# Optimization experiments

Hardware: AMD Instinct MI355X
Metric: run time of the kernel (lower is better)

The kernel has to match this reference:

```python
import jax, jax.numpy as jnp
import numpy as np

H = 512; W = 512; PH = 16; PW = 16; Q = 3; JITTER = 1e-06
NH = H // PH; NW = W // PW; P = NH * NW
B = 64


def setup_inputs() -> dict:
    key = jax.random.key(0)
    k0, k1, k2, k3, k4 = jax.random.split(key, 5)
    x = jax.random.normal(k0, (B, H, W), dtype=jnp.float32)
    logits = jax.random.normal(k1, (P, Q), dtype=jnp.float32)
    mu = jax.random.normal(k2, (P, Q, 2), dtype=jnp.float32) * 0.3
    sigma = jnp.exp(jax.random.normal(k3, (P, Q, 2), dtype=jnp.float32) * 0.3)
    bias = jax.random.normal(k4, (P, PH, PW), dtype=jnp.float32)
    return {"x": x, "logits": logits, "mu": mu, "sigma": sigma, "bias": bias}


def _make_S(logits, mu, sigma):
    # logits: (P,Q), mu/sigma: (P,Q,2) -> S: (P,PH,PW)
    w = jax.nn.softmax(logits, axis=-1)            # (P,Q)
    fy = jnp.fft.fftfreq(PH).astype(jnp.float32)   # (PH,)
    fx = jnp.fft.fftfreq(PW).astype(jnp.float32)   # (PW,)
    mu_y = mu[..., 0][:, :, None, None]            # (P,Q,1,1)
    mu_x = mu[..., 1][:, :, None, None]
    sg_y = sigma[..., 0][:, :, None, None]
    sg_x = sigma[..., 1][:, :, None, None]
    fy_b = fy[None, None, :, None]                 # (1,1,PH,1)
    fx_b = fx[None, None, None, :]                 # (1,1,1,PW)
    g1 = jnp.exp(-0.5 * (((fy_b - mu_y) / sg_y) ** 2 + ((fx_b - mu_x) / sg_x) ** 2))
    g2 = jnp.exp(-0.5 * (((fy_b + mu_y) / sg_y) ** 2 + ((fx_b + mu_x) / sg_x) ** 2))
    # weighted sum over mixture components Q
    S = jnp.einsum('pq,pqhw->phw', w, g1 + g2) + JITTER
    return S


def reference(x, logits, mu, sigma, bias):
    # x: (B,H,W) -> (B,H,W)
    S = _make_S(logits, mu, sigma)                                  # (P,PH,PW)
    x_p = x.reshape(B, NH, PH, NW, PW)
    x_p = x_p.transpose(1, 3, 0, 2, 4).reshape(P, B, PH, PW)        # (P,B,PH,PW)
    Xf = jnp.fft.fftn(x_p, axes=(-2, -1))                           # complex64
    y_p = jnp.fft.ifftn(Xf * S[:, None, :, :], axes=(-2, -1)).real  # (P,B,PH,PW)
    y_p = y_p + bias[:, None, :, :]
    y = y_p.reshape(NH, NW, B, PH, PW)
    y = y.transpose(2, 0, 3, 1, 4).reshape(B, H, W)
    return y
```

## Files before the change

kernel.cpp:

```cpp
#include <hip/hip_runtime.h>
#include <math.h>

#define HH 512
#define WW 512
#define PHH 16
#define PWW 16
#define QQ 3
#define NHH 32
#define NWW 32
#define PP 1024
#define BB 64

__device__ __forceinline__ void wfence() {
  asm volatile("" ::: "memory");
  __builtin_amdgcn_sched_barrier(0);
}

template <int SGN, int T>
__device__ __forceinline__ void bfly(float& ar, float& ai, float& br, float& bi) {
  float tr, ti;
  if constexpr (T == 0) {
    tr = br;
    ti = bi;
  } else if constexpr (T == 4) {
    if constexpr (SGN > 0) { tr = bi;  ti = -br; }
    else                   { tr = -bi; ti = br;  }
  } else if constexpr (T == 2) {
    constexpr float c = 0.70710678118654752440f;
    if constexpr (SGN > 0) { tr = c * (br + bi); ti = c * (bi - br); }
    else                   { tr = c * (br - bi); ti = c * (bi + br); }
  } else if constexpr (T == 6) {
    constexpr float c = 0.70710678118654752440f;
    if constexpr (SGN > 0) { tr = c * (bi - br);  ti = -c * (br + bi); }
    else                   { tr = -c * (br + bi); ti = c * (br - bi);  }
  } else {
    constexpr float c1 = 0.92387953251128675613f;
    constexpr float s1 = 0.38268343236508977173f;
    constexpr float wr = (T == 1) ? c1 : (T == 3) ? s1 : (T == 5) ? -s1 : -c1;
    constexpr float wi0 = (T == 1) ? -s1 : (T == 3) ? -c1 : (T == 5) ? -c1 : -s1;
    constexpr float wi = (SGN > 0) ? wi0 : -wi0;
    tr = br * wr - bi * wi;
    ti = br * wi + bi * wr;
  }
  br = ar - tr;
  bi = ai - ti;
  ar = ar + tr;
  ai = ai + ti;
}

template <int SGN>
__device__ __forceinline__ void fft16(float re[16], float im[16]) {
#define SW_(a, b)                              \
  { float t = re[a]; re[a] = re[b]; re[b] = t; \
    t = im[a]; im[a] = im[b]; im[b] = t; }
  SW_(1, 8) SW_(2, 4) SW_(3, 12) SW_(5, 10) SW_(7, 14) SW_(11, 13)
#undef SW_
#define BF_(a, b, T) bfly<SGN, T>(re[a], im[a], re[b], im[b]);
  BF_(0, 1, 0) BF_(2, 3, 0) BF_(4, 5, 0) BF_(6, 7, 0)
  BF_(8, 9, 0) BF_(10, 11, 0) BF_(12, 13, 0) BF_(14, 15, 0)
  BF_(0, 2, 0) BF_(1, 3, 4) BF_(4, 6, 0) BF_(5, 7, 4)
  BF_(8, 10, 0) BF_(9, 11, 4) BF_(12, 14, 0) BF_(13, 15, 4)
  BF_(0, 4, 0) BF_(1, 5, 2) BF_(2, 6, 4) BF_(3, 7, 6)
  BF_(8, 12, 0) BF_(9, 13, 2) BF_(10, 14, 4) BF_(11, 15, 6)
  BF_(0, 8, 0) BF_(1, 9, 1) BF_(2, 10, 2) BF_(3, 11, 3)
  BF_(4, 12, 4) BF_(5, 13, 5) BF_(6, 14, 6) BF_(7, 15, 7)
#undef BF_
}

__global__ __launch_bounds__(256, 4) void psm_kernel(
    const float* __restrict__ x, const float* __restrict__ logits,
    const float* __restrict__ mu, const float* __restrict__ sigma,
    const float* __restrict__ bias, float* __restrict__ out) {
  __shared__ float S_lds[256];
  __shared__ float tbuf[16 * 272];

  const int tid = threadIdx.x;
  const int p = blockIdx.x >> 2;
  const int b0 = (blockIdx.x & 3) << 4;
  const int g = tid >> 4;
  const int r = tid & 15;
  const int b = b0 + g;
  const int nh = p >> 5;
  const int nw = p & 31;

  {
    const int fy_i = tid >> 4;
    const int fx_i = tid & 15;
    const float fy = (float)(fy_i < 8 ? fy_i : fy_i - 16) * (1.0f / 16.0f);
    const float fx = (float)(fx_i < 8 ? fx_i : fx_i - 16) * (1.0f / 16.0f);
    const float l0 = logits[p * QQ + 0];
    const float l1 = logits[p * QQ + 1];
    const float l2 = logits[p * QQ + 2];
    const float lm = fmaxf(l0, fmaxf(l1, l2));
    const float e0 = __expf(l0 - lm);
    const float e1 = __expf(l1 - lm);
    const float e2 = __expf(l2 - lm);
    const float inv = 1.0f / (e0 + e1 + e2);
    const float wq[3] = {e0 * inv, e1 * inv, e2 * inv};
    float s = 0.0f;
#pragma unroll
    for (int q = 0; q < QQ; ++q) {
      const float muy = mu[(p * QQ + q) * 2 + 0];
      const float mux = mu[(p * QQ + q) * 2 + 1];
      const float isy = 1.0f / sigma[(p * QQ + q) * 2 + 0];
      const float isx = 1.0f / sigma[(p * QQ + q) * 2 + 1];
      const float dy1 = (fy - muy) * isy;
      const float dx1 = (fx - mux) * isx;
      const float dy2 = (fy + muy) * isy;
      const float dx2 = (fx + mux) * isx;
      const float g1 = __expf(-0.5f * (dy1 * dy1 + dx1 * dx1));
      const float g2 = __expf(-0.5f * (dy2 * dy2 + dx2 * dx2));
      s += wq[q] * (g1 + g2);
    }
    S_lds[tid] = (s + 1e-6f) * (1.0f / 256.0f);
  }
  __syncthreads();

  const size_t rowoff =
      (size_t)b * (HH * WW) + (size_t)(nh * PHH + r) * WW + (size_t)(nw * PWW);
  const float* xrow = x + rowoff;
  float re[16], im[16];
#pragma unroll
  for (int c4 = 0; c4 < 4; ++c4) {
    const float4 v = ((const float4*)xrow)[c4];
    re[c4 * 4 + 0] = v.x;
    re[c4 * 4 + 1] = v.y;
    re[c4 * 4 + 2] = v.z;
    re[c4 * 4 + 3] = v.w;
  }
#pragma unroll
  for (int c = 0; c < 16; ++c) im[c] = 0.0f;

  fft16<1>(re, im);

  float* m = &tbuf[g * 272];
#pragma unroll
  for (int c = 0; c < 16; ++c) m[r * 17 + c] = re[c];
  wfence();
#pragma unroll
  for (int k = 0; k < 16; ++k) re[k] = m[k * 17 + r];
  wfence();
#pragma unroll
  for (int c = 0; c < 16; ++c) m[r * 17 + c] = im[c];
  wfence();
#pragma unroll
  for (int k = 0; k < 16; ++k) im[k] = m[k * 17 + r];
  wfence();

  fft16<1>(re, im);
#pragma unroll
  for (int k = 0; k < 16; ++k) {
    const float s = S_lds[k * 16 + r];
    re[k] *= s;
    im[k] *= s;
  }
  fft16<-1>(re, im);

#pragma unroll
  for (int k = 0; k < 16; ++k) m[k * 17 + r] = re[k];
  wfence();
#pragma unroll
  for (int c = 0; c < 16; ++c) re[c] = m[r * 17 + c];
  wfence();
#pragma unroll
  for (int k = 0; k < 16; ++k) m[k * 17 + r] = im[k];
  wfence();
#pragma unroll
  for (int c = 0; c < 16; ++c) im[c] = m[r * 17 + c];

  fft16<-1>(re, im);

  const float* brow = bias + (size_t)p * 256 + (size_t)r * 16;
  float* orow = out + rowoff;
#pragma unroll
  for (int c4 = 0; c4 < 4; ++c4) {
    const float4 bv = ((const float4*)brow)[c4];
    float4 o;
    o.x = re[c4 * 4 + 0] + bv.x;
    o.y = re[c4 * 4 + 1] + bv.y;
    o.z = re[c4 * 4 + 2] + bv.z;
    o.w = re[c4 * 4 + 3] + bv.w;
    ((float4*)orow)[c4] = o;
  }
}

extern "C" void kernel_launch(void* const* d_in, const int* in_sizes, int n_in,
                              void* d_out, int out_size, void* d_ws,
                              size_t ws_size, hipStream_t stream) {
  (void)in_sizes;
  (void)n_in;
  (void)out_size;
  (void)d_ws;
  (void)ws_size;
  const float* x = (const float*)d_in[0];
  const float* logits = (const float*)d_in[1];
  const float* mu = (const float*)d_in[2];
  const float* sigma = (const float*)d_in[3];
  const float* bias = (const float*)d_in[4];
  float* out = (float*)d_out;

  psm_kernel<<<dim3(PP * 4), dim3(256), 0, stream>>>(x, logits, mu, sigma,
                                                     bias, out);
}
```

Baseline: 149.8 us.

## Tile blocks by image row strip with coalesced LDS-staged loads and separable filter

```diff
diff --git a/kernel.cpp b/kernel.cpp
--- a/kernel.cpp
+++ b/kernel.cpp
@@ -3,18 +3,12 @@
 
 #define HH 512
 #define WW 512
-#define PHH 16
-#define PWW 16
 #define QQ 3
-#define NHH 32
-#define NWW 32
-#define PP 1024
-#define BB 64
-
-__device__ __forceinline__ void wfence() {
-  asm volatile("" ::: "memory");
-  __builtin_amdgcn_sched_barrier(0);
-}
+
+#define SROW 260
+#define YROW 104
+
+__device__ __forceinline__ void wfence() { asm volatile("" ::: "memory"); }
 
 template <int SGN, int T>
 __device__ __forceinline__ void bfly(float& ar, float& ai, float& br, float& bi) {
@@ -67,120 +61,196 @@
 #undef BF_
 }
 
-__global__ __launch_bounds__(256, 4) void psm_kernel(
+__global__ __launch_bounds__(256) void psm_kernel(
     const float* __restrict__ x, const float* __restrict__ logits,
     const float* __restrict__ mu, const float* __restrict__ sigma,
     const float* __restrict__ bias, float* __restrict__ out) {
-  __shared__ float S_lds[256];
-  __shared__ float tbuf[16 * 272];
+  __shared__ float xs[16 * SROW];
+  __shared__ float zim[16 * SROW];
+  __shared__ float ytab[16 * YROW];
 
   const int tid = threadIdx.x;
-  const int p = blockIdx.x >> 2;
-  const int b0 = (blockIdx.x & 3) << 4;
-  const int g = tid >> 4;
+  const int bid = blockIdx.x;
+  const int half = bid & 1;
+  const int nh = (bid >> 1) & 31;
+  const int b = bid >> 6;
+
+  const size_t xbase =
+      (size_t)b * (HH * WW) + (size_t)(nh * 16) * WW + (size_t)(half * 256);
+
+  const int w = tid >> 6;
+  const int colv = tid & 63;
+
+  float4 v0, v1, v2, v3;
+  {
+    const float* src = x + xbase + (size_t)(colv * 4);
+    v0 = *(const float4*)(src + (size_t)((0 * 4 + w) * WW));
+    v1 = *(const float4*)(src + (size_t)((1 * 4 + w) * WW));
+    v2 = *(const float4*)(src + (size_t)((2 * 4 + w) * WW));
+    v3 = *(const float4*)(src + (size_t)((3 * 4 + w) * WW));
+  }
+
+  const int nwl = tid >> 4;
   const int r = tid & 15;
-  const int b = b0 + g;
-  const int nh = p >> 5;
-  const int nw = p & 31;
-
-  {
-    const int fy_i = tid >> 4;
-    const int fx_i = tid & 15;
-    const float fy = (float)(fy_i < 8 ? fy_i : fy_i - 16) * (1.0f / 16.0f);
-    const float fx = (float)(fx_i < 8 ? fx_i : fx_i - 16) * (1.0f / 16.0f);
-    const float l0 = logits[p * QQ + 0];
-    const float l1 = logits[p * QQ + 1];
-    const float l2 = logits[p * QQ + 2];
+  const int pg = nh * 32 + half * 16 + nwl;
+
+  {
+    const float fyr = (float)(r < 8 ? r : r - 16) * (1.0f / 16.0f);
+#pragma unroll
+    for (int m = 0; m < 6; ++m) {
+      const int q = m >> 1;
+      const float muy = mu[(pg * QQ + q) * 2 + 0];
+      const float isy = 1.0f / sigma[(pg * QQ + q) * 2 + 0];
+      const float d = ((m & 1) ? (fyr + muy) : (fyr - muy)) * isy;
+      ytab[nwl * YROW + m * 16 + r] = __expf(-0.5f * d * d);
+    }
+  }
+
+  {
+    float* dst = &xs[colv * 4];
+    *(float4*)(dst + (0 * 4 + w) * SROW) = v0;
+    *(float4*)(dst + (1 * 4 + w) * SROW) = v1;
+    *(float4*)(dst + (2 * 4 + w) * SROW) = v2;
+    *(float4*)(dst + (3 * 4 + w) * SROW) = v3;
+  }
+  __syncthreads();
+
+  float re[16], im[16];
+  {
+    const float* rb = &xs[r * SROW + nwl * 16];
+#pragma unroll
+    for (int c4 = 0; c4 < 4; ++c4) {
+      const float4 t = *(const float4*)(rb + c4 * 4);
+      re[c4 * 4 + 0] = t.x;
+      re[c4 * 4 + 1] = t.y;
+      re[c4 * 4 + 2] = t.z;
+      re[c4 * 4 + 3] = t.w;
+    }
+  }
+#pragma unroll
+  for (int c = 0; c < 16; ++c) im[c] = 0.0f;
+  fft16<1>(re, im);
+  {
+    float* rbr = &xs[r * SROW + nwl * 16];
+    float* rbi = &zim[r * SROW + nwl * 16];
+#pragma unroll
+    for (int c4 = 0; c4 < 4; ++c4) {
+      float4 a, bb;
+      a.x = re[c4 * 4 + 0]; a.y = re[c4 * 4 + 1];
+      a.z = re[c4 * 4 + 2]; a.w = re[c4 * 4 + 3];
+      bb.x = im[c4 * 4 + 0]; bb.y = im[c4 * 4 + 1];
+      bb.z = im[c4 * 4 + 2]; bb.w = im[c4 * 4 + 3];
+      *(float4*)(rbr + c4 * 4) = a;
+      *(float4*)(rbi + c4 * 4) = bb;
+    }
+  }
+  wfence();
+
+  float s[16];
+  {
+    const float fxk = (float)(r < 8 ? r : r - 16) * (1.0f / 16.0f);
+    const float l0 = logits[pg * QQ + 0];
+    const float l1 = logits[pg * QQ + 1];
+    const float l2 = logits[pg * QQ + 2];
     const float lm = fmaxf(l0, fmaxf(l1, l2));
     const float e0 = __expf(l0 - lm);
     const float e1 = __expf(l1 - lm);
     const float e2 = __expf(l2 - lm);
-    const float inv = 1.0f / (e0 + e1 + e2);
-    const float wq[3] = {e0 * inv, e1 * inv, e2 * inv};
-    float s = 0.0f;
-#pragma unroll
-    for (int q = 0; q < QQ; ++q) {
-      const float muy = mu[(p * QQ + q) * 2 + 0];
-      const float mux = mu[(p * QQ + q) * 2 + 1];
-      const float isy = 1.0f / sigma[(p * QQ + q) * 2 + 0];
-      const float isx = 1.0f / sigma[(p * QQ + q) * 2 + 1];
-      const float dy1 = (fy - muy) * isy;
-      const float dx1 = (fx - mux) * isx;
-      const float dy2 = (fy + muy) * isy;
-      const float dx2 = (fx + mux) * isx;
-      const float g1 = __expf(-0.5f * (dy1 * dy1 + dx1 * dx1));
-      const float g2 = __expf(-0.5f * (dy2 * dy2 + dx2 * dx2));
-      s += wq[q] * (g1 + g2);
-    }
-    S_lds[tid] = (s + 1e-6f) * (1.0f / 256.0f);
+    const float inv = (1.0f / 256.0f) / (e0 + e1 + e2);
+    float ax[6];
+#pragma unroll
+    for (int m = 0; m < 6; ++m) {
+      const int q = m >> 1;
+      const float mux = mu[(pg * QQ + q) * 2 + 1];
+      const float isx = 1.0f / sigma[(pg * QQ + q) * 2 + 1];
+      const float d = ((m & 1) ? (fxk + mux) : (fxk - mux)) * isx;
+      const float wqv = ((q == 0) ? e0 : (q == 1) ? e1 : e2) * inv;
+      ax[m] = wqv * __expf(-0.5f * d * d);
+    }
+    const float* yt = &ytab[nwl * YROW];
+#pragma unroll
+    for (int j4 = 0; j4 < 4; ++j4) {
+      const float4 a0 = *(const float4*)(yt + 0 * 16 + j4 * 4);
+      const float4 a1 = *(const float4*)(yt + 1 * 16 + j4 * 4);
+      const float4 a2 = *(const float4*)(yt + 2 * 16 + j4 * 4);
+      const float4 a3 = *(const float4*)(yt + 3 * 16 + j4 * 4);
+      const float4 a4 = *(const float4*)(yt + 4 * 16 + j4 * 4);
+      const float4 a5 = *(const float4*)(yt + 5 * 16 + j4 * 4);
+      s[j4 * 4 + 0] = a0.x * ax[0] + a1.x * ax[1] + a2.x * ax[2] +
+                      a3.x * ax[3] + a4.x * ax[4] + a5.x * ax[5] + 3.90625e-9f;
+      s[j4 * 4 + 1] = a0.y * ax[0] + a1.y * ax[1] + a2.y * ax[2] +
+                      a3.y * ax[3] + a4.y * ax[4] + a5.y * ax[5] + 3.90625e-9f;
+      s[j4 * 4 + 2] = a0.z * ax[0] + a1.z * ax[1] + a2.z * ax[2] +
+                      a3.z * ax[3] + a4.z * ax[4] + a5.z * ax[5] + 3.90625e-9f;
+      s[j4 * 4 + 3] = a0.w * ax[0] + a1.w * ax[1] + a2.w * ax[2] +
+                      a3.w * ax[3] + a4.w * ax[4] + a5.w * ax[5] + 3.90625e-9f;
+    }
+  }
+  {
+    const float* cbr = &xs[nwl * 16 + r];
+    const float* cbi = &zim[nwl * 16 + r];
+#pragma unroll
+    for (int j = 0; j < 16; ++j) {
+      re[j] = cbr[j * SROW];
+      im[j] = cbi[j * SROW];
+    }
+  }
+  fft16<1>(re, im);
+#pragma unroll
+  for (int j = 0; j < 16; ++j) {
+    re[j] *= s[j];
+    im[j] *= s[j];
+  }
+  fft16<-1>(re, im);
+  {
+    float* cbr = &xs[nwl * 16 + r];
+    float* cbi = &zim[nwl * 16 + r];
+#pragma unroll
+    for (int j = 0; j < 16; ++j) {
+      cbr[j * SROW] = re[j];
+      cbi[j * SROW] = im[j];
+    }
+  }
+  wfence();
+
+  {
+    const float* rbr = &xs[r * SROW + nwl * 16];
+    const float* rbi = &zim[r * SROW + nwl * 16];
+#pragma unroll
+    for (int c4 = 0; c4 < 4; ++c4) {
+      const float4 t = *(const float4*)(rbr + c4 * 4);
+      const float4 u = *(const float4*)(rbi + c4 * 4);
+      re[c4 * 4 + 0] = t.x; re[c4 * 4 + 1] = t.y;
+      re[c4 * 4 + 2] = t.z; re[c4 * 4 + 3] = t.w;
+      im[c4 * 4 + 0] = u.x; im[c4 * 4 + 1] = u.y;
+      im[c4 * 4 + 2] = u.z; im[c4 * 4 + 3] = u.w;
+    }
+  }
+  fft16<-1>(re, im);
+  {
+    const float* brow = bias + (size_t)pg * 256 + (size_t)(r * 16);
+    float* rbo = &zim[r * SROW + nwl * 16];
+#pragma unroll
+    for (int c4 = 0; c4 < 4; ++c4) {
+      const float4 bv = *(const float4*)(brow + c4 * 4);
+      float4 o;
+      o.x = re[c4 * 4 + 0] + bv.x;
+      o.y = re[c4 * 4 + 1] + bv.y;
+      o.z = re[c4 * 4 + 2] + bv.z;
+      o.w = re[c4 * 4 + 3] + bv.w;
+      *(float4*)(rbo + c4 * 4) = o;
+    }
   }
   __syncthreads();
 
-  const size_t rowoff =
-      (size_t)b * (HH * WW) + (size_t)(nh * PHH + r) * WW + (size_t)(nw * PWW);
-  const float* xrow = x + rowoff;
-  float re[16], im[16];
-#pragma unroll
-  for (int c4 = 0; c4 < 4; ++c4) {
-    const float4 v = ((const float4*)xrow)[c4];
-    re[c4 * 4 + 0] = v.x;
-    re[c4 * 4 + 1] = v.y;
-    re[c4 * 4 + 2] = v.z;
-    re[c4 * 4 + 3] = v.w;
-  }
-#pragma unroll
-  for (int c = 0; c < 16; ++c) im[c] = 0.0f;
-
-  fft16<1>(re, im);
-
-  float* m = &tbuf[g * 272];
-#pragma unroll
-  for (int c = 0; c < 16; ++c) m[r * 17 + c] = re[c];
-  wfence();
-#pragma unroll
-  for (int k = 0; k < 16; ++k) re[k] = m[k * 17 + r];
-  wfence();
-#pragma unroll
-  for (int c = 0; c < 16; ++c) m[r * 17 + c] = im[c];
-  wfence();
-#pragma unroll
-  for (int k = 0; k < 16; ++k) im[k] = m[k * 17 + r];
-  wfence();
-
-  fft16<1>(re, im);
-#pragma unroll
-  for (int k = 0; k < 16; ++k) {
-    const float s = S_lds[k * 16 + r];
-    re[k] *= s;
-    im[k] *= s;
-  }
-  fft16<-1>(re, im);
-
-#pragma unroll
-  for (int k = 0; k < 16; ++k) m[k * 17 + r] = re[k];
-  wfence();
-#pragma unroll
-  for (int c = 0; c < 16; ++c) re[c] = m[r * 17 + c];
-  wfence();
-#pragma unroll
-  for (int k = 0; k < 16; ++k) m[k * 17 + r] = im[k];
-  wfence();
-#pragma unroll
-  for (int c = 0; c < 16; ++c) im[c] = m[r * 17 + c];
-
-  fft16<-1>(re, im);
-
-  const float* brow = bias + (size_t)p * 256 + (size_t)r * 16;
-  float* orow = out + rowoff;
-#pragma unroll
-  for (int c4 = 0; c4 < 4; ++c4) {
-    const float4 bv = ((const float4*)brow)[c4];
-    float4 o;
-    o.x = re[c4 * 4 + 0] + bv.x;
-    o.y = re[c4 * 4 + 1] + bv.y;
-    o.z = re[c4 * 4 + 2] + bv.z;
-    o.w = re[c4 * 4 + 3] + bv.w;
-    ((float4*)orow)[c4] = o;
+  {
+    float* dst = out + xbase + (size_t)(colv * 4);
+    const float* srcl = &zim[colv * 4];
+#pragma unroll
+    for (int j = 0; j < 4; ++j) {
+      const float4 t = *(const float4*)(srcl + (j * 4 + w) * SROW);
+      *(float4*)(dst + (size_t)((j * 4 + w) * WW)) = t;
+    }
   }
 }
 
@@ -199,6 +269,6 @@
   const float* bias = (const float*)d_in[4];
   float* out = (float*)d_out;
 
-  psm_kernel<<<dim3(PP * 4), dim3(256), 0, stream>>>(x, logits, mu, sigma,
-                                                     bias, out);
-}
+  psm_kernel<<<dim3(64 * 32 * 2), dim3(256), 0, stream>>>(x, logits, mu, sigma,
+                                                          bias, out);
+}
```

Measured after the change: 133.0 us. -11.3%, faster.
